# Performance work log

Measured on AMD Instinct MI355X. Metric: run time of the kernel, lower is better.

## Reference

```python
import jax, jax.numpy as jnp
import numpy as np

N_SEQ, BS, E, H = 2048, 8, 512, 8
HD = E // H  # 64


def setup_inputs() -> dict:
    key = jax.random.key(0)
    k1, k2, k3 = jax.random.split(key, 3)
    seq = jax.random.normal(k1, (N_SEQ, BS, E), dtype=jnp.float32)
    # xavier_uniform for Linear(E, 3E): bound = sqrt(6/(fan_in+fan_out))
    b_qkv_w = float(np.sqrt(6.0 / (E + 3 * E)))
    W_qkv = jax.random.uniform(k2, (3 * E, E), minval=-b_qkv_w, maxval=b_qkv_w, dtype=jnp.float32)
    b_out_w = float(np.sqrt(6.0 / (E + E)))
    W_out = jax.random.uniform(k3, (E, E), minval=-b_out_w, maxval=b_out_w, dtype=jnp.float32)
    b_qkv = jnp.zeros((3 * E,), dtype=jnp.float32)
    b_out = jnp.zeros((E,), dtype=jnp.float32)
    return {"seq": seq, "W_qkv": W_qkv, "b_qkv": b_qkv, "W_out": W_out, "b_out": b_out}


def reference(seq, W_qkv, b_qkv, W_out, b_out):
    n, bs, e = seq.shape
    # fused QKV projection: [n, bs, 3E]
    qkv = jnp.einsum('nbe,fe->nbf', seq, W_qkv) + b_qkv
    # [n, bs, 3, H, HD] -> q/k/v each [n, bs*H, HD] (bs outer, H inner)
    qkv = qkv.reshape(n, bs, 3, H, HD)
    q = qkv[:, :, 0].reshape(n, bs * H, HD)
    k = qkv[:, :, 1].reshape(n, bs * H, HD)
    v = qkv[:, :, 2].reshape(n, bs * H, HD)
    scale = 1.0 / jnp.sqrt(jnp.asarray(HD, dtype=seq.dtype))
    # full [bs*H, n, n] score matrix as in the original
    attn = jnp.einsum('qbd,kbd->bqk', q * scale, k)
    attn = jax.nn.softmax(attn, axis=-1)
    out = jnp.einsum('bqk,kbd->qbd', attn, v)  # [n, bs*H, HD]
    out = out.reshape(n, bs, e)
    return jnp.einsum('nbe,fe->nbf', out, W_out) + b_out
```

## Files before the change

### kernel.cpp

```cpp
#include <hip/hip_runtime.h>
#include <stdint.h>

typedef unsigned short ushort_t;
typedef unsigned int uint32;
typedef __attribute__((ext_vector_type(8))) short short8;
typedef __attribute__((ext_vector_type(4))) float f32x4;
typedef __attribute__((ext_vector_type(16))) float f32x16;
typedef __attribute__((ext_vector_type(4))) uint32 uint4v;

#define NSEQ 2048
#define BSZ 8
#define EMB 512
#define NHEAD 8
#define HDIM 64
#define MTOK (NSEQ*BSZ)
#define NH_TOT (BSZ*NHEAD)
#define NP (NSEQ/128)

#define VMCNT0 asm volatile("s_waitcnt vmcnt(0)" ::: "memory")
#define BAR __builtin_amdgcn_s_barrier()

__device__ __forceinline__ ushort_t f2bf(float f) {
  uint32_t u = __builtin_bit_cast(uint32_t, f);
  u += 0x7FFFu + ((u >> 16) & 1u);
  return (ushort_t)(u >> 16);
}
__device__ __forceinline__ float bf2f(ushort_t u) {
  uint32_t x = ((uint32_t)u) << 16;
  return __builtin_bit_cast(float, x);
}

__device__ __forceinline__ void gll16(const void* g, void* l) {
  __builtin_amdgcn_global_load_lds(
      (const __attribute__((address_space(1))) void*)g,
      (__attribute__((address_space(3))) void*)l, 16, 0, 0);
}

__device__ __forceinline__ int SW(int r) { return (r & 7) ^ ((r >> 3) & 7); }

__global__ void cvt3(const float* __restrict__ a, ushort_t* __restrict__ oa, int na4,
                     const float* __restrict__ b, ushort_t* __restrict__ ob, int nb4,
                     const float* __restrict__ c, ushort_t* __restrict__ oc, int nc4) {
  int i = blockIdx.x * blockDim.x + threadIdx.x;
  const float* src; ushort_t* dst; int j = i;
  if (j < na4) { src = a; dst = oa; }
  else {
    j -= na4;
    if (j < nb4) { src = b; dst = ob; }
    else { j -= nb4; if (j >= nc4) return; src = c; dst = oc; }
  }
  float4 v = reinterpret_cast<const float4*>(src)[j];
  union { ushort_t u[4]; uint64_t q; } o;
  o.u[0] = f2bf(v.x); o.u[1] = f2bf(v.y); o.u[2] = f2bf(v.z); o.u[3] = f2bf(v.w);
  reinterpret_cast<uint64_t*>(dst)[j] = o.q;
}

template<int MODE>
__global__ __launch_bounds__(256) void gemm_bt(
    const ushort_t* __restrict__ A, const ushort_t* __restrict__ B,
    const float* __restrict__ bias,
    float* __restrict__ Cf, ushort_t* __restrict__ Cq, ushort_t* __restrict__ VTq,
    int M, int N, int K)
{
  __shared__ __align__(16) ushort_t SH[2][128*64];
  ushort_t* As = &SH[0][0];
  ushort_t* Bs = &SH[1][0];
  const int t = threadIdx.x;
  const int w = t >> 6, l = t & 63;

  const int nbx = gridDim.x;
  const int bid = blockIdx.x + nbx * blockIdx.y;
  const int per = (nbx * gridDim.y) >> 3;
  const int swz = (bid & 7) * per + (bid >> 3);
  const int tm = (swz / nbx) * 128, tn = (swz % nbx) * 128;
  const int wm = w >> 1, wn = w & 1;

  f32x4 acc[4][4] = {};

  for (int k0 = 0; k0 < K; k0 += 64) {
    #pragma unroll
    for (int j = 0; j < 4; ++j) {
      int row = j*32 + w*8 + (l >> 3);
      int cole = ((l & 7) * 8) ^ ((row & 7) << 3);
      const ushort_t* ga = A + (size_t)(tm + row) * K + k0 + cole;
      const ushort_t* gb = B + (size_t)(tn + row) * K + k0 + cole;
      gll16(ga, As + j*2048 + w*512 + l*8);
      gll16(gb, Bs + j*2048 + w*512 + l*8);
    }
    __syncthreads();
    #pragma unroll
    for (int kk = 0; kk < 2; ++kk) {
      short8 af[4], bfr[4];
      #pragma unroll
      for (int mi = 0; mi < 4; ++mi) {
        int row = wm*64 + mi*16 + (l & 15);
        int byte = row*128 + ((kk*64 + ((l >> 4) * 16)) ^ ((row & 7) << 4));
        af[mi] = *reinterpret_cast<const short8*>(reinterpret_cast<const char*>(As) + byte);
      }
      #pragma unroll
      for (int ni = 0; ni < 4; ++ni) {
        int row = wn*64 + ni*16 + (l & 15);
        int byte = row*128 + ((kk*64 + ((l >> 4) * 16)) ^ ((row & 7) << 4));
        bfr[ni] = *reinterpret_cast<const short8*>(reinterpret_cast<const char*>(Bs) + byte);
      }
      #pragma unroll
      for (int mi = 0; mi < 4; ++mi)
        #pragma unroll
        for (int ni = 0; ni < 4; ++ni)
          acc[mi][ni] = __builtin_amdgcn_mfma_f32_16x16x32_bf16(af[mi], bfr[ni], acc[mi][ni], 0, 0, 0);
    }
    __syncthreads();
  }

  if (MODE == 0 && tn >= 2*EMB) {
    ushort_t* T = &SH[0][0];
    #pragma unroll
    for (int mi = 0; mi < 4; ++mi) {
      #pragma unroll
      for (int ni = 0; ni < 4; ++ni) {
        #pragma unroll
        for (int r = 0; r < 4; ++r) {
          int rowl = wm*64 + mi*16 + ((l >> 4) * 4) + r;
          int coll = wn*64 + ni*16 + (l & 15);
          float v = acc[mi][ni][r] + bias[tn + coll];
          int b = rowl & 7, nloc = rowl >> 3;
          int hx = coll >> 6, hd = coll & 63;
          int rowT = (hx*8 + b)*64 + hd;
          int pc = (nloc >> 3) ^ (rowT & 1);
          T[rowT*16 + pc*8 + (nloc & 7)] = f2bf(v);
        }
      }
    }
    __syncthreads();
    const int hxg0 = (tn >> 6) & 7;
    #pragma unroll
    for (int i = 0; i < 8; ++i) {
      int c = i*256 + t;
      int rowT = c >> 1, lc = c & 1;
      int pc = lc ^ (rowT & 1);
      short8 val = *reinterpret_cast<const short8*>(&T[rowT*16 + pc*8]);
      int hx = rowT >> 9;
      int b  = (rowT >> 6) & 7;
      int hd = rowT & 63;
      int head = b*NHEAD + hxg0 + hx;
      size_t n = (size_t)(tm >> 3) + lc*8;
      *reinterpret_cast<short8*>(VTq + (size_t)head * HDIM * NSEQ + (size_t)hd * NSEQ + n) = val;
    }
    return;
  }

  #pragma unroll
  for (int mi = 0; mi < 4; ++mi) {
    #pragma unroll
    for (int ni = 0; ni < 4; ++ni) {
      #pragma unroll
      for (int r = 0; r < 4; ++r) {
        int row = tm + wm*64 + mi*16 + ((l >> 4) * 4) + r;
        int col = tn + wn*64 + ni*16 + (l & 15);
        float v = acc[mi][ni][r] + bias[col];
        if constexpr (MODE == 1) {
          Cf[(size_t)row * N + col] = v;
        } else {
          int w3 = col >> 9, hx = (col >> 6) & 7, hd = col & 63;
          int n = row >> 3, bb = row & 7;
          Cq[(size_t)w3 * ((size_t)NH_TOT * NSEQ * HDIM)
             + ((size_t)(bb * NHEAD + hx) * NSEQ + n) * HDIM + hd] = f2bf(v);
        }
      }
    }
  }
}

#define CSC 0.18033688011112042f

__global__ __launch_bounds__(256, 2) void attn_fwd(
    const ushort_t* __restrict__ Qb, const ushort_t* __restrict__ Kb,
    const ushort_t* __restrict__ VTb, ushort_t* __restrict__ Ob)
{
  __shared__ __align__(16) ushort_t Ks[2][2][64*64];
  __shared__ __align__(16) ushort_t Vs[2][2][64*64];
  const int t = threadIdx.x, w = t >> 6, l = t & 63;
  const int lq = l & 31, h = l >> 5;
  const int L = blockIdx.x + 8 * blockIdx.y;
  const int Tid = (L & 7) * 64 + (L >> 3);
  const int bh = Tid >> 3, qt = Tid & 7;
  const int b = bh >> 3, hh = bh & 7;
  const size_t hbase  = (size_t)bh * NSEQ * HDIM;
  const size_t vtbase = (size_t)bh * HDIM * NSEQ;
  const int qbase = qt*256 + w*64;

  short8 qreg[2][4];
  #pragma unroll
  for (int qb = 0; qb < 2; ++qb)
    #pragma unroll
    for (int kd = 0; kd < 4; ++kd) {
      short8 raw = *reinterpret_cast<const short8*>(
          Qb + hbase + (size_t)(qbase + qb*32 + lq) * HDIM + kd*16 + h*8);
      short8 q;
      #pragma unroll
      for (int e = 0; e < 8; ++e)
        q[e] = (short)f2bf(bf2f((ushort_t)raw[e]) * CSC);
      qreg[qb][kd] = q;
    }

  f32x16 Oacc[2][2] = {};
  f32x16 lacc0 = {}, lacc1 = {};

  const short ONE = (short)0x3F80;
  short8 ones = { ONE, ONE, ONE, ONE, ONE, ONE, ONE, ONE };

  const int srow = t >> 3;
  const int scol = (t & 7) * 8;
  const int c0 = scol ^ (SW(srow) << 3);
  const int c1 = scol ^ (SW(srow + 32) << 3);
  const ushort_t* Kg0 = Kb  + hbase  + (size_t)srow       * HDIM + c0;
  const ushort_t* Kg1 = Kb  + hbase  + (size_t)(srow+32)  * HDIM + c1;
  const ushort_t* Vg0 = VTb + vtbase + (size_t)srow       * NSEQ + c0;
  const ushort_t* Vg1 = VTb + vtbase + (size_t)(srow+32)  * NSEQ + c1;

  auto STAGE = [&](int bi, int p) {
    #pragma unroll
    for (int ss = 0; ss < 2; ++ss) {
      int kt = p*2 + ss;
      size_t ko = (size_t)kt * 64 * HDIM;
      int    vo = kt * 64;
      gll16(Kg0 + ko, &Ks[bi][ss][0]    + t*8);
      gll16(Kg1 + ko, &Ks[bi][ss][2048] + t*8);
      gll16(Vg0 + vo, &Vs[bi][ss][0]    + t*8);
      gll16(Vg1 + vo, &Vs[bi][ss][2048] + t*8);
    }
  };

  VMCNT0;
  STAGE(0, 0);

  int cur = 0;
  #pragma unroll 1
  for (int p = 0; p < NP; ++p) {
    VMCNT0;
    BAR;
    if (p + 1 < NP) STAGE(cur ^ 1, p + 1);

    #pragma unroll
    for (int ss = 0; ss < 2; ++ss) {
      const char* KsC = reinterpret_cast<const char*>(&Ks[cur][ss][0]);
      const char* VsC = reinterpret_cast<const char*>(&Vs[cur][ss][0]);

      short8 kf[2][4];
      #pragma unroll
      for (int rp = 0; rp < 2; ++rp) {
        int row = rp*32 + lq;
        int swr = SW(row) << 4;
        #pragma unroll
        for (int kd = 0; kd < 4; ++kd)
          kf[rp][kd] = *reinterpret_cast<const short8*>(
              KsC + row*128 + ((kd*32 + h*16) ^ swr));
      }

      uint32 pa0[4][4], pa1[4][4];

      {
        f32x16 s0 = {}, s1 = {};
        __builtin_amdgcn_s_setprio(1);
        #pragma unroll
        for (int kd = 0; kd < 4; ++kd) {
          s0 = __builtin_amdgcn_mfma_f32_32x32x16_bf16(kf[0][kd], qreg[0][kd], s0, 0, 0, 0);
          s1 = __builtin_amdgcn_mfma_f32_32x32x16_bf16(kf[1][kd], qreg[0][kd], s1, 0, 0, 0);
        }
        __builtin_amdgcn_s_setprio(0);
        #pragma unroll
        for (int r = 0; r < 16; ++r) {
          s0[r] = __builtin_amdgcn_exp2f(s0[r]);
          s1[r] = __builtin_amdgcn_exp2f(s1[r]);
        }
        uint32 w0[8], w1[8];
        #pragma unroll
        for (int i = 0; i < 8; ++i) {
          float a0 = s0[2*i], b0 = s0[2*i+1];
          float a1 = s1[2*i], b1 = s1[2*i+1];
          asm("v_cvt_pk_bf16_f32 %0, %1, %2" : "=v"(w0[i]) : "v"(a0), "v"(b0));
          asm("v_cvt_pk_bf16_f32 %0, %1, %2" : "=v"(w1[i]) : "v"(a1), "v"(b1));
        }
        #pragma unroll
        for (int sg = 0; sg < 2; ++sg) {
          uint32 a, bb;
          a = w0[4*sg+0]; bb = w0[4*sg+2];
          asm("v_permlane32_swap_b32 %0, %1" : "+v"(a), "+v"(bb));
          pa0[sg][0] = a; pa0[sg][2] = bb;
          a = w0[4*sg+1]; bb = w0[4*sg+3];
          asm("v_permlane32_swap_b32 %0, %1" : "+v"(a), "+v"(bb));
          pa0[sg][1] = a; pa0[sg][3] = bb;
          a = w1[4*sg+0]; bb = w1[4*sg+2];
          asm("v_permlane32_swap_b32 %0, %1" : "+v"(a), "+v"(bb));
          pa0[2+sg][0] = a; pa0[2+sg][2] = bb;
          a = w1[4*sg+1]; bb = w1[4*sg+3];
          asm("v_permlane32_swap_b32 %0, %1" : "+v"(a), "+v"(bb));
          pa0[2+sg][1] = a; pa0[2+sg][3] = bb;
        }
      }

      {
        f32x16 s0 = {}, s1 = {};
        __builtin_amdgcn_s_setprio(1);
        #pragma unroll
        for (int kd = 0; kd < 4; ++kd) {
          s0 = __builtin_amdgcn_mfma_f32_32x32x16_bf16(kf[0][kd], qreg[1][kd], s0, 0, 0, 0);
          s1 = __builtin_amdgcn_mfma_f32_32x32x16_bf16(kf[1][kd], qreg[1][kd], s1, 0, 0, 0);
        }
        __builtin_amdgcn_s_setprio(0);
        #pragma unroll
        for (int r = 0; r < 16; ++r) {
          s0[r] = __builtin_amdgcn_exp2f(s0[r]);
          s1[r] = __builtin_amdgcn_exp2f(s1[r]);
        }
        uint32 w0[8], w1[8];
        #pragma unroll
        for (int i = 0; i < 8; ++i) {
          float a0 = s0[2*i], b0 = s0[2*i+1];
          float a1 = s1[2*i], b1 = s1[2*i+1];
          asm("v_cvt_pk_bf16_f32 %0, %1, %2" : "=v"(w0[i]) : "v"(a0), "v"(b0));
          asm("v_cvt_pk_bf16_f32 %0, %1, %2" : "=v"(w1[i]) : "v"(a1), "v"(b1));
        }
        #pragma unroll
        for (int sg = 0; sg < 2; ++sg) {
          uint32 a, bb;
          a = w0[4*sg+0]; bb = w0[4*sg+2];
          asm("v_permlane32_swap_b32 %0, %1" : "+v"(a), "+v"(bb));
          pa1[sg][0] = a; pa1[sg][2] = bb;
          a = w0[4*sg+1]; bb = w0[4*sg+3];
          asm("v_permlane32_swap_b32 %0, %1" : "+v"(a), "+v"(bb));
          pa1[sg][1] = a; pa1[sg][3] = bb;
          a = w1[4*sg+0]; bb = w1[4*sg+2];
          asm("v_permlane32_swap_b32 %0, %1" : "+v"(a), "+v"(bb));
          pa1[2+sg][0] = a; pa1[2+sg][2] = bb;
          a = w1[4*sg+1]; bb = w1[4*sg+3];
          asm("v_permlane32_swap_b32 %0, %1" : "+v"(a), "+v"(bb));
          pa1[2+sg][1] = a; pa1[2+sg][3] = bb;
        }
      }

      short8 vf[2][4];
      #pragma unroll
      for (int dt = 0; dt < 2; ++dt) {
        int d = dt*32 + lq;
        int swd = SW(d) << 4;
        #pragma unroll
        for (int km = 0; km < 4; ++km)
          vf[dt][km] = *reinterpret_cast<const short8*>(
              VsC + d*128 + ((km*32 + h*16) ^ swd));
      }

      __builtin_amdgcn_s_setprio(1);
      #pragma unroll
      for (int km = 0; km < 4; ++km) {
        uint4v u0; u0[0] = pa0[km][0]; u0[1] = pa0[km][1]; u0[2] = pa0[km][2]; u0[3] = pa0[km][3];
        short8 paf0 = __builtin_bit_cast(short8, u0);
        uint4v u1; u1[0] = pa1[km][0]; u1[1] = pa1[km][1]; u1[2] = pa1[km][2]; u1[3] = pa1[km][3];
        short8 paf1 = __builtin_bit_cast(short8, u1);
        Oacc[0][0] = __builtin_amdgcn_mfma_f32_32x32x16_bf16(paf0, vf[0][km], Oacc[0][0], 0, 0, 0);
        lacc0      = __builtin_amdgcn_mfma_f32_32x32x16_bf16(paf0, ones,     lacc0,      0, 0, 0);
        Oacc[0][1] = __builtin_amdgcn_mfma_f32_32x32x16_bf16(paf0, vf[1][km], Oacc[0][1], 0, 0, 0);
        Oacc[1][0] = __builtin_amdgcn_mfma_f32_32x32x16_bf16(paf1, vf[0][km], Oacc[1][0], 0, 0, 0);
        lacc1      = __builtin_amdgcn_mfma_f32_32x32x16_bf16(paf1, ones,     lacc1,      0, 0, 0);
        Oacc[1][1] = __builtin_amdgcn_mfma_f32_32x32x16_bf16(paf1, vf[1][km], Oacc[1][1], 0, 0, 0);
      }
      __builtin_amdgcn_s_setprio(0);
    }

    cur ^= 1;
  }

  #pragma unroll
  for (int r = 0; r < 16; ++r) {
    int qrow = (r & 3) + 8*(r >> 2) + 4*h;
    float li0 = __builtin_amdgcn_rcpf(lacc0[r]);
    float li1 = __builtin_amdgcn_rcpf(lacc1[r]);
    #pragma unroll
    for (int dt = 0; dt < 2; ++dt) {
      int d = dt*32 + lq;
      int n0 = qbase + qrow;
      int n1 = qbase + 32 + qrow;
      Ob[((size_t)n0 * BSZ + b) * EMB + hh*64 + d] = f2bf(Oacc[0][dt][r] * li0);
      Ob[((size_t)n1 * BSZ + b) * EMB + hh*64 + d] = f2bf(Oacc[1][dt][r] * li1);
    }
  }
}

extern "C" void kernel_launch(void* const* d_in, const int* in_sizes, int n_in,
                              void* d_out, int out_size, void* d_ws, size_t ws_size,
                              hipStream_t stream) {
  (void)in_sizes; (void)n_in; (void)out_size; (void)ws_size;
  const float* seq  = (const float*)d_in[0];
  const float* Wqkv = (const float*)d_in[1];
  const float* bqkv = (const float*)d_in[2];
  const float* Wout = (const float*)d_in[3];
  const float* bout = (const float*)d_in[4];
  float* out = (float*)d_out;

  ushort_t* seq_bf  = (ushort_t*)d_ws;
  ushort_t* wqkv_bf = seq_bf  + (size_t)MTOK * EMB;
  ushort_t* wout_bf = wqkv_bf + (size_t)3 * EMB * EMB;
  ushort_t* qkvbuf  = wout_bf + (size_t)EMB * EMB;
  ushort_t* vtbuf   = qkvbuf  + (size_t)3 * NH_TOT * NSEQ * HDIM;
  ushort_t* attno   = qkvbuf  + (size_t)2 * NH_TOT * NSEQ * HDIM;

  const int na4 = MTOK*EMB/4, nb4 = 3*EMB*EMB/4, nc4 = EMB*EMB/4;
  cvt3<<<(na4+nb4+nc4 + 255)/256, 256, 0, stream>>>(
      seq, seq_bf, na4, Wqkv, wqkv_bf, nb4, Wout, wout_bf, nc4);

  gemm_bt<0><<<dim3(12, 128), 256, 0, stream>>>(seq_bf, wqkv_bf, bqkv, nullptr, qkvbuf,
                                                vtbuf, MTOK, 3*EMB, EMB);

  const ushort_t* Qb  = qkvbuf;
  const ushort_t* Kb  = qkvbuf + (size_t)NH_TOT * NSEQ * HDIM;

  attn_fwd<<<dim3(8, 64), 256, 0, stream>>>(Qb, Kb, vtbuf, attno);

  gemm_bt<1><<<dim3(4, 128), 256, 0, stream>>>(attno, wout_bf, bout, out, nullptr,
                                               nullptr, MTOK, EMB, EMB);
}
```

Measured before the change: 153.0 us.

## Rewrite QKV GEMM with 256x256 tiles, 512 threads, double-buffered LDS prefetch

Replaces the templated QKV projection GEMM with a dedicated kernel that uses 256x256 output tiles, 8 waves and 128KB of dynamic shared memory. It double-buffers the K-loop so the next stage's global-to-LDS loads are issued while the current stage computes, and it raises wave priority around the MFMA bursts. The goal is more reuse per tile and hiding global load latency. In exchange the grid is smaller (384 blocks), occupancy is lower, and there are extra barriers inside the compute loop.

```diff
diff --git a/kernel.cpp b/kernel.cpp
--- a/kernel.cpp
+++ b/kernel.cpp
@@ -55,16 +55,153 @@
   reinterpret_cast<uint64_t*>(dst)[j] = o.q;
 }
 
-template<int MODE>
-__global__ __launch_bounds__(256) void gemm_bt(
+__global__ __launch_bounds__(512) void gemm_qkv(
     const ushort_t* __restrict__ A, const ushort_t* __restrict__ B,
     const float* __restrict__ bias,
-    float* __restrict__ Cf, ushort_t* __restrict__ Cq, ushort_t* __restrict__ VTq,
+    ushort_t* __restrict__ Cq, ushort_t* __restrict__ VTq)
+{
+  extern __shared__ __align__(16) ushort_t SH[];
+  const int t = threadIdx.x;
+  const int l = t & 63;
+  const int w = t >> 6;
+  const int wm = w >> 2, wn = w & 3;
+
+  const int bid = blockIdx.x;
+  const int swz = (bid & 7) * 48 + (bid >> 3);
+  const int tm = (swz / 6) * 256, tn = (swz % 6) * 256;
+
+  f32x4 acc[8][4] = {};
+
+  auto STAGE = [&](int buf, int k) {
+    #pragma unroll
+    for (int h = 0; h < 2; ++h) {
+      #pragma unroll
+      for (int j = 0; j < 2; ++j) {
+        int idx = j*512 + t;
+        int row = idx >> 3, slot = idx & 7;
+        int cole = (slot*8) ^ ((row & 7) * 8);
+        gll16(A + (size_t)(tm + h*128 + row) * EMB + k*64 + cole,
+              SH + (size_t)(h)*8192 + (size_t)buf*16384 + idx*8);
+        gll16(B + (size_t)(tn + h*128 + row) * EMB + k*64 + cole,
+              SH + 32768 + (size_t)(h)*8192 + (size_t)buf*16384 + idx*8);
+      }
+    }
+  };
+
+  STAGE(0, 0);
+
+  #pragma unroll 2
+  for (int k = 0; k < 8; ++k) {
+    VMCNT0;
+    BAR;
+    if (k + 1 < 8) STAGE((k + 1) & 1, k + 1);
+
+    const char* Ah = reinterpret_cast<const char*>(
+        SH + (size_t)wm*8192 + (size_t)(k & 1)*16384);
+    const char* Bh = reinterpret_cast<const char*>(
+        SH + 32768 + (size_t)(wn >> 1)*8192 + (size_t)(k & 1)*16384);
+
+    short8 bfr[4][2];
+    #pragma unroll
+    for (int ni = 0; ni < 4; ++ni) {
+      int row = (wn & 1)*64 + ni*16 + (l & 15);
+      #pragma unroll
+      for (int ks = 0; ks < 2; ++ks) {
+        int byte = row*128 + ((ks*64 + ((l >> 4) * 16)) ^ ((row & 7) << 4));
+        bfr[ni][ks] = *reinterpret_cast<const short8*>(Bh + byte);
+      }
+    }
+
+    #pragma unroll
+    for (int q = 0; q < 4; ++q) {
+      short8 af[2][2];
+      #pragma unroll
+      for (int i = 0; i < 2; ++i) {
+        int row = (q*2 + i)*16 + (l & 15);
+        #pragma unroll
+        for (int ks = 0; ks < 2; ++ks) {
+          int byte = row*128 + ((ks*64 + ((l >> 4) * 16)) ^ ((row & 7) << 4));
+          af[i][ks] = *reinterpret_cast<const short8*>(Ah + byte);
+        }
+      }
+      BAR;
+      __builtin_amdgcn_s_setprio(1);
+      #pragma unroll
+      for (int i = 0; i < 2; ++i)
+        #pragma unroll
+        for (int ni = 0; ni < 4; ++ni)
+          #pragma unroll
+          for (int ks = 0; ks < 2; ++ks)
+            acc[q*2 + i][ni] = __builtin_amdgcn_mfma_f32_16x16x32_bf16(
+                af[i][ks], bfr[ni][ks], acc[q*2 + i][ni], 0, 0, 0);
+      __builtin_amdgcn_s_setprio(0);
+      BAR;
+    }
+  }
+
+  if (tn >= 2*EMB) {
+    ushort_t* T = SH;
+    #pragma unroll
+    for (int mi = 0; mi < 8; ++mi) {
+      #pragma unroll
+      for (int ni = 0; ni < 4; ++ni) {
+        #pragma unroll
+        for (int r = 0; r < 4; ++r) {
+          int rowl = wm*128 + mi*16 + ((l >> 4) * 4) + r;
+          int coll = wn*64 + ni*16 + (l & 15);
+          float v = acc[mi][ni][r] + bias[tn + coll];
+          int hxl = coll >> 6, hd = coll & 63;
+          int b = rowl & 7, nloc = rowl >> 3;
+          int rowT = (hxl*8 + b)*64 + hd;
+          int pc = (nloc >> 3) ^ (rowT & 3);
+          T[rowT*32 + pc*8 + (nloc & 7)] = f2bf(v);
+        }
+      }
+    }
+    __syncthreads();
+    const int hx0 = (tn >> 6) & 7;
+    #pragma unroll
+    for (int i = 0; i < 16; ++i) {
+      int c = i*512 + t;
+      int rowT = c >> 2, lc = c & 3;
+      int pc = lc ^ (rowT & 3);
+      short8 val = *reinterpret_cast<const short8*>(T + rowT*32 + pc*8);
+      int hxl = rowT >> 9;
+      int b   = (rowT >> 6) & 7;
+      int hd  = rowT & 63;
+      int head = b*NHEAD + hx0 + hxl;
+      size_t n = (size_t)(tm >> 3) + lc*8;
+      *reinterpret_cast<short8*>(VTq + (size_t)head * HDIM * NSEQ
+                                 + (size_t)hd * NSEQ + n) = val;
+    }
+    return;
+  }
+
+  #pragma unroll
+  for (int mi = 0; mi < 8; ++mi) {
+    #pragma unroll
+    for (int ni = 0; ni < 4; ++ni) {
+      #pragma unroll
+      for (int r = 0; r < 4; ++r) {
+        int row = tm + wm*128 + mi*16 + ((l >> 4) * 4) + r;
+        int col = tn + wn*64 + ni*16 + (l & 15);
+        float v = acc[mi][ni][r] + bias[col];
+        int w3 = col >> 9, hx = (col >> 6) & 7, hd = col & 63;
+        int n = row >> 3, bb = row & 7;
+        Cq[(size_t)w3 * ((size_t)NH_TOT * NSEQ * HDIM)
+           + ((size_t)(bb * NHEAD + hx) * NSEQ + n) * HDIM + hd] = f2bf(v);
+      }
+    }
+  }
+}
+
+__global__ __launch_bounds__(256) void gemm_out(
+    const ushort_t* __restrict__ A, const ushort_t* __restrict__ B,
+    const float* __restrict__ bias, float* __restrict__ Cf,
     int M, int N, int K)
 {
-  __shared__ __align__(16) ushort_t SH[2][128*64];
-  ushort_t* As = &SH[0][0];
-  ushort_t* Bs = &SH[1][0];
+  __shared__ __align__(16) ushort_t As[128*64];
+  __shared__ __align__(16) ushort_t Bs[128*64];
   const int t = threadIdx.x;
   const int w = t >> 6, l = t & 63;
 
@@ -82,10 +219,8 @@
     for (int j = 0; j < 4; ++j) {
       int row = j*32 + w*8 + (l >> 3);
       int cole = ((l & 7) * 8) ^ ((row & 7) << 3);
-      const ushort_t* ga = A + (size_t)(tm + row) * K + k0 + cole;
-      const ushort_t* gb = B + (size_t)(tn + row) * K + k0 + cole;
-      gll16(ga, As + j*2048 + w*512 + l*8);
-      gll16(gb, Bs + j*2048 + w*512 + l*8);
+      gll16(A + (size_t)(tm + row) * K + k0 + cole, As + j*2048 + w*512 + l*8);
+      gll16(B + (size_t)(tn + row) * K + k0 + cole, Bs + j*2048 + w*512 + l*8);
     }
     __syncthreads();
     #pragma unroll
@@ -112,63 +247,16 @@
     __syncthreads();
   }
 
-  if (MODE == 0 && tn >= 2*EMB) {
-    ushort_t* T = &SH[0][0];
-    #pragma unroll
-    for (int mi = 0; mi < 4; ++mi) {
-      #pragma unroll
-      for (int ni = 0; ni < 4; ++ni) {
-        #pragma unroll
-        for (int r = 0; r < 4; ++r) {
-          int rowl = wm*64 + mi*16 + ((l >> 4) * 4) + r;
-          int coll = wn*64 + ni*16 + (l & 15);
-          float v = acc[mi][ni][r] + bias[tn + coll];
-          int b = rowl & 7, nloc = rowl >> 3;
-          int hx = coll >> 6, hd = coll & 63;
-          int rowT = (hx*8 + b)*64 + hd;
-          int pc = (nloc >> 3) ^ (rowT & 1);
-          T[rowT*16 + pc*8 + (nloc & 7)] = f2bf(v);
-        }
-      }
-    }
-    __syncthreads();
-    const int hxg0 = (tn >> 6) & 7;
-    #pragma unroll
-    for (int i = 0; i < 8; ++i) {
-      int c = i*256 + t;
-      int rowT = c >> 1, lc = c & 1;
-      int pc = lc ^ (rowT & 1);
-      short8 val = *reinterpret_cast<const short8*>(&T[rowT*16 + pc*8]);
-      int hx = rowT >> 9;
-      int b  = (rowT >> 6) & 7;
-      int hd = rowT & 63;
-      int head = b*NHEAD + hxg0 + hx;
-      size_t n = (size_t)(tm >> 3) + lc*8;
-      *reinterpret_cast<short8*>(VTq + (size_t)head * HDIM * NSEQ + (size_t)hd * NSEQ + n) = val;
-    }
-    return;
-  }
-
   #pragma unroll
-  for (int mi = 0; mi < 4; ++mi) {
-    #pragma unroll
-    for (int ni = 0; ni < 4; ++ni) {
+  for (int mi = 0; mi < 4; ++mi)
+    #pragma unroll
+    for (int ni = 0; ni < 4; ++ni)
       #pragma unroll
       for (int r = 0; r < 4; ++r) {
         int row = tm + wm*64 + mi*16 + ((l >> 4) * 4) + r;
         int col = tn + wn*64 + ni*16 + (l & 15);
-        float v = acc[mi][ni][r] + bias[col];
-        if constexpr (MODE == 1) {
-          Cf[(size_t)row * N + col] = v;
-        } else {
-          int w3 = col >> 9, hx = (col >> 6) & 7, hd = col & 63;
-          int n = row >> 3, bb = row & 7;
-          Cq[(size_t)w3 * ((size_t)NH_TOT * NSEQ * HDIM)
-             + ((size_t)(bb * NHEAD + hx) * NSEQ + n) * HDIM + hd] = f2bf(v);
-        }
-      }
-    }
-  }
+        Cf[(size_t)row * N + col] = acc[mi][ni][r] + bias[col];
+      }
 }
 
 #define CSC 0.18033688011112042f
@@ -408,14 +496,19 @@
   cvt3<<<(na4+nb4+nc4 + 255)/256, 256, 0, stream>>>(
       seq, seq_bf, na4, Wqkv, wqkv_bf, nb4, Wout, wout_bf, nc4);
 
-  gemm_bt<0><<<dim3(12, 128), 256, 0, stream>>>(seq_bf, wqkv_bf, bqkv, nullptr, qkvbuf,
-                                                vtbuf, MTOK, 3*EMB, EMB);
+  static int attr_set = 0;
+  if (!attr_set) {
+    hipFuncSetAttribute((const void*)gemm_qkv,
+                        hipFuncAttributeMaxDynamicSharedMemorySize, 131072);
+    attr_set = 1;
+  }
+  gemm_qkv<<<384, 512, 131072, stream>>>(seq_bf, wqkv_bf, bqkv, qkvbuf, vtbuf);
 
   const ushort_t* Qb  = qkvbuf;
   const ushort_t* Kb  = qkvbuf + (size_t)NH_TOT * NSEQ * HDIM;
 
   attn_fwd<<<dim3(8, 64), 256, 0, stream>>>(Qb, Kb, vtbuf, attno);
 
-  gemm_bt<1><<<dim3(4, 128), 256, 0, stream>>>(attno, wout_bf, bout, out, nullptr,
-                                               nullptr, MTOK, EMB, EMB);
-}
+  gemm_out<<<dim3(4, 128), 256, 0, stream>>>(attno, wout_bf, bout, out,
+                                             MTOK, EMB, EMB);
+}
```

Measured after the change: 151.4 us. Within noise of the previous version (-1.0%).

## Double-buffer LDS tiles in projection GEMM to overlap loads with MFMA

Applied to the files above, without the earlier changes.

The projection GEMM now keeps two LDS buffers for A and B. It prefetches the next K-slice with global-to-LDS loads while MFMAs run on the current slice, replacing the old load, sync, compute, sync loop with one barrier per iteration. It also raises wave priority around the MFMA block and adds a two-blocks-per-CU launch bound. The cost is twice the LDS per block (64KB), which may reduce occupancy. The epilogue transpose buffer is moved to As[0].

```diff
diff --git a/kernel.cpp b/kernel.cpp
--- a/kernel.cpp
+++ b/kernel.cpp
@@ -56,15 +56,14 @@
 }
 
 template<int MODE>
-__global__ __launch_bounds__(256) void gemm_bt(
+__global__ __launch_bounds__(256, 2) void gemm_bt(
     const ushort_t* __restrict__ A, const ushort_t* __restrict__ B,
     const float* __restrict__ bias,
     float* __restrict__ Cf, ushort_t* __restrict__ Cq, ushort_t* __restrict__ VTq,
     int M, int N, int K)
 {
-  __shared__ __align__(16) ushort_t SH[2][128*64];
-  ushort_t* As = &SH[0][0];
-  ushort_t* Bs = &SH[1][0];
+  __shared__ __align__(16) ushort_t As[2][128*64];
+  __shared__ __align__(16) ushort_t Bs[2][128*64];
   const int t = threadIdx.x;
   const int w = t >> 6, l = t & 63;
 
@@ -77,17 +76,28 @@
 
   f32x4 acc[4][4] = {};
 
-  for (int k0 = 0; k0 < K; k0 += 64) {
+  auto STAGE = [&](int buf, int k0) {
     #pragma unroll
     for (int j = 0; j < 4; ++j) {
       int row = j*32 + w*8 + (l >> 3);
       int cole = ((l & 7) * 8) ^ ((row & 7) << 3);
-      const ushort_t* ga = A + (size_t)(tm + row) * K + k0 + cole;
-      const ushort_t* gb = B + (size_t)(tn + row) * K + k0 + cole;
-      gll16(ga, As + j*2048 + w*512 + l*8);
-      gll16(gb, Bs + j*2048 + w*512 + l*8);
-    }
-    __syncthreads();
+      gll16(A + (size_t)(tm + row) * K + k0 + cole, &As[buf][0] + j*2048 + w*512 + l*8);
+      gll16(B + (size_t)(tn + row) * K + k0 + cole, &Bs[buf][0] + j*2048 + w*512 + l*8);
+    }
+  };
+
+  const int NK = K >> 6;
+  STAGE(0, 0);
+
+  int cur = 0;
+  #pragma unroll 1
+  for (int k = 0; k < NK; ++k) {
+    VMCNT0;
+    BAR;
+    if (k + 1 < NK) STAGE(cur ^ 1, (k + 1) << 6);
+
+    const char* AsC = reinterpret_cast<const char*>(&As[cur][0]);
+    const char* BsC = reinterpret_cast<const char*>(&Bs[cur][0]);
     #pragma unroll
     for (int kk = 0; kk < 2; ++kk) {
       short8 af[4], bfr[4];
@@ -95,25 +105,27 @@
       for (int mi = 0; mi < 4; ++mi) {
         int row = wm*64 + mi*16 + (l & 15);
         int byte = row*128 + ((kk*64 + ((l >> 4) * 16)) ^ ((row & 7) << 4));
-        af[mi] = *reinterpret_cast<const short8*>(reinterpret_cast<const char*>(As) + byte);
+        af[mi] = *reinterpret_cast<const short8*>(AsC + byte);
       }
       #pragma unroll
       for (int ni = 0; ni < 4; ++ni) {
         int row = wn*64 + ni*16 + (l & 15);
         int byte = row*128 + ((kk*64 + ((l >> 4) * 16)) ^ ((row & 7) << 4));
-        bfr[ni] = *reinterpret_cast<const short8*>(reinterpret_cast<const char*>(Bs) + byte);
-      }
+        bfr[ni] = *reinterpret_cast<const short8*>(BsC + byte);
+      }
+      __builtin_amdgcn_s_setprio(1);
       #pragma unroll
       for (int mi = 0; mi < 4; ++mi)
         #pragma unroll
         for (int ni = 0; ni < 4; ++ni)
           acc[mi][ni] = __builtin_amdgcn_mfma_f32_16x16x32_bf16(af[mi], bfr[ni], acc[mi][ni], 0, 0, 0);
-    }
-    __syncthreads();
+      __builtin_amdgcn_s_setprio(0);
+    }
+    cur ^= 1;
   }
 
   if (MODE == 0 && tn >= 2*EMB) {
-    ushort_t* T = &SH[0][0];
+    ushort_t* T = &As[0][0];
     #pragma unroll
     for (int mi = 0; mi < 4; ++mi) {
       #pragma unroll
```

Measured after the change: 152.4 us. About the same (-0.4%).
